# Optimization experiments

Measured on AMD Instinct MI355X. Metric: run time of the kernel, lower is better.

Reference implementation:

```python
import jax, jax.numpy as jnp
import numpy as np

NUM_STEPS = 100
STEP = 2.0 / (NUM_STEPS - 1)          # bin width over [-1, 1]
EPS = 1.0 / NUM_STEPS
TSIZE = NUM_STEPS                      # bin centers t_k = -1 + k*STEP, k=0..99
B, D = 4096, 128
NUM_CLASSES = 100


def setup_inputs() -> dict:
    key = jax.random.key(0)
    k1, k2 = jax.random.split(key)
    embeddings = jax.random.normal(k1, (B, D), dtype=jnp.float32)
    classes = jax.random.randint(k2, (B,), 0, NUM_CLASSES)
    return {"embeddings": embeddings, "classes": classes}


def _histogram_loss(embeddings, classes):
    n = embeddings.shape[0]
    iu, ju = np.triu_indices(n, 1)            # static upper-triangular pair indices
    # cosine similarity of all pairs (outer_cosine_similarity)
    en = embeddings / jnp.linalg.norm(embeddings, axis=1, keepdims=True)
    dists = en @ en.T                          # [B, B]
    s = jnp.clip(dists[iu, ju], -1.0 + 1e-6, 1.0 - 1e-6)   # [P]
    pos = (classes[iu] == classes[ju])         # [P] bool

    # soft triangular-kernel 2-bin scatter (equivalent to indsa/indsb masking):
    # bin j gets (t_j + STEP - s)/STEP, bin j+1 gets (s - t_j)/STEP
    j = jnp.floor((s + 1.0 - 1e-6) / STEP).astype(jnp.int32)   # lower bin index
    t_j = j.astype(s.dtype) * STEP - 1.0
    w_hi = (s - t_j) / STEP                    # weight for bin j+1
    w_lo = (t_j + STEP - s) / STEP             # weight for bin j

    def histogram(mask):
        m = mask.astype(s.dtype)
        size = m.sum()
        h = jnp.zeros((TSIZE,), dtype=s.dtype)
        h = h.at[j].add(w_lo * m).at[j + 1].add(w_hi * m)
        return h / size

    hist_pos = histogram(pos)
    hist_neg = histogram(~pos)
    # tril-masked repeat + sum(0) in the original is exactly a cumulative sum
    hist_pos_cdf = jnp.cumsum(hist_pos)
    return jnp.sum(hist_neg * hist_pos_cdf)


def reference(embeddings, classes):
    return _histogram_loss(embeddings, classes)
```

## Files before the change

### kernel.cpp

```cpp
#include <hip/hip_runtime.h>
#include <hip/hip_bf16.h>
#include <cstddef>

#define BN 4096
#define DD 128
#define NSTEPS 100
#define PTILE 128
#define PLSTR 136
#define GRID_T 32
#define NOFF 496
#define NBLK2 512
#define NREPH 16
#define NREPC2 8

typedef __attribute__((ext_vector_type(8))) short bf16x8;
typedef __attribute__((ext_vector_type(4))) float f32x4;

__device__ __forceinline__ void faddf(float* p, float v) { unsafeAtomicAdd(p, v); }

#define ZERON 166

__global__ __launch_bounds__(256) void hl_normalize(const float* __restrict__ emb,
                                                    ushort* __restrict__ out,
                                                    float* __restrict__ zero_blk) {
    if (blockIdx.x == 0 && threadIdx.x < ZERON) zero_blk[threadIdx.x] = 0.f;
    int w = threadIdx.x >> 6;
    int lane = threadIdx.x & 63;
    int row = (blockIdx.x << 2) + w;
    const float2 v = *(const float2*)(emb + (size_t)row * DD + 2 * lane);
    float ss = v.x * v.x + v.y * v.y;
    #pragma unroll
    for (int off = 32; off > 0; off >>= 1) ss += __shfl_xor(ss, off);
    float inv = 1.0f / sqrtf(ss);
    __hip_bfloat16 b0 = __float2bfloat16(v.x * inv);
    __hip_bfloat16 b1 = __float2bfloat16(v.y * inv);
    ushort2 pk;
    pk.x = *(ushort*)&b0;
    pk.y = *(ushort*)&b1;
    *(ushort2*)(out + (size_t)row * DD + 2 * lane) = pk;
}

__global__ __launch_bounds__(256) void hl_poscls(const ushort* __restrict__ nemb,
                                                 const int* __restrict__ cls,
                                                 float* __restrict__ gPos,
                                                 unsigned int* __restrict__ gDoneP,
                                                 float* __restrict__ gCdf) {
    const int c = blockIdx.x;
    __shared__ int idx[256];
    __shared__ int scan[256];
    __shared__ ushort As[64 * PLSTR];
    __shared__ ushort Bs[64 * PLSTR];
    __shared__ float hpos[NREPH * 101];
    __shared__ int mTot;
    __shared__ int lastFlag;
    const int tid = threadIdx.x;

    for (int i = tid; i < NREPH * 101; i += 256) hpos[i] = 0.f;

    const int base = tid * 16;
    int myCnt = 0;
    #pragma unroll
    for (int k = 0; k < 16; ++k) myCnt += (cls[base + k] == c);
    scan[tid] = myCnt;
    __syncthreads();
    for (int s = 1; s < 256; s <<= 1) {
        int v = (tid >= s) ? scan[tid - s] : 0;
        __syncthreads();
        scan[tid] += v;
        __syncthreads();
    }
    int w = scan[tid] - myCnt;
    if (tid == 255) mTot = scan[255] > 256 ? 256 : scan[255];
    #pragma unroll
    for (int k = 0; k < 16; ++k) {
        if (cls[base + k] == c && w < 256) { idx[w] = base + k; ++w; }
    }
    __syncthreads();
    const int m = mTot;
    const int nt = (m + 63) >> 6;

    constexpr float INVSTEP = 49.5f;
    constexpr float CLIPV = 1.0f - 1e-6f;

    const int lane = tid & 63;
    const int wv = tid >> 6;
    const int lr = lane & 15;
    const int kg = lane >> 4;
    const int rep = (lane & 15) * 101;

    for (int si = 0; si < nt; ++si) {
        for (int sj = si; sj < nt; ++sj) {
            __syncthreads();
            #pragma unroll
            for (int it = 0; it < 4; ++it) {
                int q = it * 256 + tid;
                int row = q >> 4;
                int ch = q & 15;
                int ga = si * 64 + row;
                int gb = sj * 64 + row;
                int ra = idx[ga < m ? ga : 0];
                int rb = idx[gb < m ? gb : 0];
                *(float4*)(&As[row * PLSTR + ch * 8]) =
                    *(const float4*)(nemb + (size_t)ra * DD + ch * 8);
                *(float4*)(&Bs[row * PLSTR + ch * 8]) =
                    *(const float4*)(nemb + (size_t)rb * DD + ch * 8);
            }
            __syncthreads();

            f32x4 zero4 = {0.f, 0.f, 0.f, 0.f};
            f32x4 pacc[4] = {zero4, zero4, zero4, zero4};
            #pragma unroll
            for (int ks = 0; ks < 4; ++ks) {
                bf16x8 af = *(const bf16x8*)(&As[(wv * 16 + lr) * PLSTR + ks * 32 + kg * 8]);
                #pragma unroll
                for (int fb = 0; fb < 4; ++fb) {
                    bf16x8 bf = *(const bf16x8*)(&Bs[(fb * 16 + lr) * PLSTR + ks * 32 + kg * 8]);
                    pacc[fb] = __builtin_amdgcn_mfma_f32_16x16x32_bf16(af, bf, pacc[fb], 0, 0, 0);
                }
            }

            #pragma unroll
            for (int fb = 0; fb < 4; ++fb) {
                const int gb = sj * 64 + fb * 16 + lr;
                #pragma unroll
                for (int j = 0; j < 4; ++j) {
                    const int ga = si * 64 + wv * 16 + kg * 4 + j;
                    if (ga < gb && gb < m) {
                        float s = pacc[fb][j];
                        s = fminf(fmaxf(s, -CLIPV), CLIPV);
                        float u = (s + CLIPV) * INVSTEP;
                        int jb = (int)u;
                        if (jb > 98) jb = 98;
                        float w_hi = u - (float)jb;
                        float w_lo = 1.0f - w_hi;
                        faddf(&hpos[rep + jb], w_lo);
                        faddf(&hpos[rep + jb + 1], w_hi);
                    }
                }
            }
        }
    }
    __syncthreads();
    if (tid < NSTEPS) {
        float v = 0.f;
        #pragma unroll
        for (int r = 0; r < NREPH; ++r) v += hpos[r * 101 + tid];
        if (v != 0.f) faddf(&gPos[tid], v);
    }
    __threadfence();
    if (tid == 0) {
        unsigned int tk = atomicAdd(gDoneP, 1u);
        lastFlag = (tk == NSTEPS - 1);
    }
    __syncthreads();
    if (lastFlag) {
        float v = (tid < NSTEPS)
            ? __hip_atomic_load(&gPos[tid], __ATOMIC_RELAXED, __HIP_MEMORY_SCOPE_AGENT) : 0.f;
        if (tid < 128) hpos[tid] = v;
        __syncthreads();
        for (int off = 1; off < 128; off <<= 1) {
            float x = 0.f;
            if (tid < 128 && tid >= off) x = hpos[tid - off];
            __syncthreads();
            if (tid < 128) hpos[tid] += x;
            __syncthreads();
        }
        const float invsp = 1.0f / hpos[NSTEPS - 1];
        if (tid < NSTEPS) gCdf[tid] = hpos[tid] * invsp;
    }
}

__global__ __launch_bounds__(256, 2) void hl_neg(const ushort* __restrict__ nemb,
                                                 const int* __restrict__ cls,
                                                 const float* __restrict__ gCdf,
                                                 float* __restrict__ gLoss,
                                                 float* __restrict__ gCnt,
                                                 unsigned int* __restrict__ gDone,
                                                 float* __restrict__ out) {
    __shared__ __align__(16) char arena[65536];
    ushort* As = (ushort*)arena;
    ushort* Bs = (ushort*)(arena + 32768);
    float* accL = (float*)arena;
    __shared__ float2 cdf2[NREPC2 * 101];
    __shared__ float red[8];
    __shared__ int clsA[PTILE], clsB[PTILE];

    const int tid = threadIdx.x;
    const int lane = tid & 63;
    const int wid = tid >> 6;
    const int wr = wid >> 1, wc = wid & 1;
    const int lr = lane & 15;
    const int kg = lane >> 4;

    int ti0, tj0, ti1 = 0, nu = 1;
    {
        int t = blockIdx.x;
        if (t < NOFF) {
            int ti = 0, rem = t;
            while (rem >= GRID_T - 1 - ti) { rem -= GRID_T - 1 - ti; ++ti; }
            ti0 = ti; tj0 = ti + 1 + rem;
        } else {
            int d = (t - NOFF) * 2;
            ti0 = tj0 = d; ti1 = d + 1; nu = 2;
        }
    }

    for (int i = tid; i < NREPC2 * NSTEPS; i += 256) {
        int r = i / NSTEPS, b = i - r * NSTEPS;
        float c0 = gCdf[b];
        float c1 = gCdf[(b < NSTEPS - 1) ? b + 1 : NSTEPS - 1];
        float2 cd; cd.x = c0; cd.y = c1 - c0;
        cdf2[r * 101 + b] = cd;
    }

    constexpr float INVSTEP = 49.5f;
    constexpr float CLIPV = 1.0f - 1e-6f;
    const float2* crep2 = &cdf2[(lane & 7) * 101];
    const int li_base = wr * 64 + (kg << 2);
    const int lj_base = wc * 64 + lr;

    float lacc = 0.f, lcnt = 0.f;
    const int rloc = lane >> 4;
    const int pch = lane & 15;

    for (int u = 0; u < nu; ++u) {
        const int ti = u ? ti1 : ti0;
        const int tj = u ? ti1 : tj0;
        const bool diag = (ti == tj);

        __syncthreads();
        if (tid < PTILE) clsA[tid] = cls[ti * PTILE + tid];
        else             clsB[tid - PTILE] = cls[tj * PTILE + (tid - PTILE)];

        {
            const ushort* Ag = nemb + (size_t)(ti * PTILE) * DD;
            const ushort* Bg = nemb + (size_t)(tj * PTILE) * DD;
            #pragma unroll
            for (int t = 0; t < 8; ++t) {
                int row = wid * 32 + t * 4 + rloc;
                int lch = pch ^ (row & 7);
                const ushort* ga = Ag + (size_t)row * DD + lch * 8;
                ushort* la = &As[(wid * 32 + t * 4) * 128];
                __builtin_amdgcn_global_load_lds(
                    (const __attribute__((address_space(1))) void*)ga,
                    (__attribute__((address_space(3))) void*)la, 16, 0, 0);
            }
            if (!diag) {
                #pragma unroll
                for (int t = 0; t < 8; ++t) {
                    int row = wid * 32 + t * 4 + rloc;
                    int lch = pch ^ (row & 7);
                    const ushort* gb = Bg + (size_t)row * DD + lch * 8;
                    ushort* lb = &Bs[(wid * 32 + t * 4) * 128];
                    __builtin_amdgcn_global_load_lds(
                        (const __attribute__((address_space(1))) void*)gb,
                        (__attribute__((address_space(3))) void*)lb, 16, 0, 0);
                }
            }
        }
        __syncthreads();

        const ushort* Bsel = diag ? As : Bs;
        const int* clsBsel = diag ? clsA : clsB;

        f32x4 zero4 = {0.f, 0.f, 0.f, 0.f};
        f32x4 acc[4][4];
        #pragma unroll
        for (int a = 0; a < 4; ++a)
            #pragma unroll
            for (int b = 0; b < 4; ++b) acc[a][b] = zero4;

        #pragma unroll
        for (int ks = 0; ks < 4; ++ks) {
            bf16x8 af[4], bfr[4];
            #pragma unroll
            for (int f = 0; f < 4; ++f) {
                int arow = wr * 64 + f * 16 + lr;
                int pca = ((ks << 2) | kg) ^ (arow & 7);
                af[f] = *(const bf16x8*)(&As[arow * 128 + pca * 8]);
                int brow = wc * 64 + f * 16 + lr;
                int pcb = ((ks << 2) | kg) ^ (brow & 7);
                bfr[f] = *(const bf16x8*)(&Bsel[brow * 128 + pcb * 8]);
            }
            #pragma unroll
            for (int fa = 0; fa < 4; ++fa)
                #pragma unroll
                for (int fb = 0; fb < 4; ++fb)
                    acc[fa][fb] = __builtin_amdgcn_mfma_f32_16x16x32_bf16(af[fa], bfr[fb], acc[fa][fb], 0, 0, 0);
        }

        __syncthreads();

        #pragma unroll
        for (int fb = 0; fb < 4; ++fb)
            #pragma unroll
            for (int fa = 0; fa < 4; ++fa)
                #pragma unroll
                for (int j = 0; j < 4; ++j)
                    accL[(fb * 16 + fa * 4 + j) * 256 + tid] = acc[fa][fb][j];
        __syncthreads();

        const bool offdiag = !diag;
        #pragma unroll 1
        for (int p = 0; p < 64; ++p) {
            const int fb = p >> 4, fa = (p >> 2) & 3, j = p & 3;
            const int li = li_base + fa * 16 + j;
            const int lj = lj_base + fb * 16;
            float s = accL[p * 256 + tid];
            int ca = clsA[li];
            int cb = clsBsel[lj];
            const bool mneg = (offdiag || (li < lj)) && (ca != cb);
            s = fminf(fmaxf(s, -CLIPV), CLIPV);
            float uu = (s + CLIPV) * INVSTEP;
            int jb = (int)uu;
            if (jb > 98) jb = 98;
            float w_hi = uu - (float)jb;
            float2 cd = crep2[jb];
            float mm = mneg ? 1.0f : 0.0f;
            lacc = fmaf(mm, fmaf(w_hi, cd.y, cd.x), lacc);
            lcnt += mm;
        }
    }

    #pragma unroll
    for (int off = 32; off > 0; off >>= 1) {
        lacc += __shfl_xor(lacc, off);
        lcnt += __shfl_xor(lcnt, off);
    }
    if (lane == 0) { red[wid] = lacc; red[4 + wid] = lcnt; }
    __syncthreads();
    if (tid == 0) {
        float L = red[0] + red[1] + red[2] + red[3];
        float C = red[4] + red[5] + red[6] + red[7];
        faddf(&gLoss[blockIdx.x & 31], L);
        faddf(&gCnt[blockIdx.x & 31], C);
        __threadfence();
        unsigned int tk = atomicAdd(gDone, 1u);
        if (tk == NBLK2 - 1) {
            __threadfence();
            float ls = 0.f, cs = 0.f;
            for (int i = 0; i < 32; ++i) {
                ls += __hip_atomic_load(&gLoss[i], __ATOMIC_RELAXED, __HIP_MEMORY_SCOPE_AGENT);
                cs += __hip_atomic_load(&gCnt[i], __ATOMIC_RELAXED, __HIP_MEMORY_SCOPE_AGENT);
            }
            out[0] = ls / cs;
        }
    }
}

extern "C" void kernel_launch(void* const* d_in, const int* in_sizes, int n_in,
                              void* d_out, int out_size, void* d_ws, size_t ws_size,
                              hipStream_t stream) {
    const float* emb = (const float*)d_in[0];
    const int* classes = (const int*)d_in[1];
    float* out = (float*)d_out;

    ushort* nemb = (ushort*)d_ws;
    float* ctl = (float*)((char*)d_ws + (size_t)BN * DD * sizeof(ushort));
    float* gPos = ctl;
    float* gLoss = gPos + NSTEPS;
    float* gCnt = gLoss + 32;
    unsigned int* gDone = (unsigned int*)(gCnt + 32);
    unsigned int* gDoneP = gDone + 1;
    float* gCdf = (float*)(gDoneP + 1);

    hl_normalize<<<BN / 4, 256, 0, stream>>>(emb, nemb, ctl);
    hl_poscls<<<NSTEPS, 256, 0, stream>>>(nemb, classes, gPos, gDoneP, gCdf);
    hl_neg<<<NBLK2, 256, 0, stream>>>(nemb, classes, gCdf, gLoss, gCnt, gDone, out);
}
```

Measured before the change: 51.64 us.

## Process two tile pairs per block, prefetch second tile, epilogue from registers

Each hl_neg block now handles two tile-pair units, with the grid halved to 264 blocks. The second unit's global-to-LDS loads are issued right after the first unit's MFMAs finish, so they overlap the first unit's epilogue. The epilogue reads similarities straight from the MFMA accumulator registers instead of spilling them to LDS and re-reading, which removes one barrier and the LDS round trip. The cost is more register pressure and fewer blocks, which with 256 CUs leaves roughly one block per CU.

```diff
diff --git a/kernel.cpp b/kernel.cpp
--- a/kernel.cpp
+++ b/kernel.cpp
@@ -9,7 +9,8 @@
 #define PLSTR 136
 #define GRID_T 32
 #define NOFF 496
-#define NBLK2 512
+#define NUNITS 528
+#define NBLK 264
 #define NREPH 16
 #define NREPC2 8
 
@@ -177,13 +178,11 @@
                                                  float* __restrict__ gCnt,
                                                  unsigned int* __restrict__ gDone,
                                                  float* __restrict__ out) {
-    __shared__ __align__(16) char arena[65536];
-    ushort* As = (ushort*)arena;
-    ushort* Bs = (ushort*)(arena + 32768);
-    float* accL = (float*)arena;
+    __shared__ ushort As[PTILE * 128];
+    __shared__ ushort Bs[PTILE * 128];
     __shared__ float2 cdf2[NREPC2 * 101];
     __shared__ float red[8];
-    __shared__ int clsA[PTILE], clsB[PTILE];
+    __shared__ int clsAb[2][PTILE], clsBb[2][PTILE];
 
     const int tid = threadIdx.x;
     const int lane = tid & 63;
@@ -192,16 +191,16 @@
     const int lr = lane & 15;
     const int kg = lane >> 4;
 
-    int ti0, tj0, ti1 = 0, nu = 1;
-    {
-        int t = blockIdx.x;
-        if (t < NOFF) {
-            int ti = 0, rem = t;
+    int tiU[2], tjU[2];
+    #pragma unroll
+    for (int u = 0; u < 2; ++u) {
+        int id = blockIdx.x * 2 + u;
+        if (id < NOFF) {
+            int ti = 0, rem = id;
             while (rem >= GRID_T - 1 - ti) { rem -= GRID_T - 1 - ti; ++ti; }
-            ti0 = ti; tj0 = ti + 1 + rem;
+            tiU[u] = ti; tjU[u] = ti + 1 + rem;
         } else {
-            int d = (t - NOFF) * 2;
-            ti0 = tj0 = d; ti1 = d + 1; nu = 2;
+            tiU[u] = tjU[u] = id - NOFF;
         }
     }
 
@@ -223,45 +222,47 @@
     const int rloc = lane >> 4;
     const int pch = lane & 15;
 
-    for (int u = 0; u < nu; ++u) {
-        const int ti = u ? ti1 : ti0;
-        const int tj = u ? ti1 : tj0;
-        const bool diag = (ti == tj);
-
-        __syncthreads();
-        if (tid < PTILE) clsA[tid] = cls[ti * PTILE + tid];
-        else             clsB[tid - PTILE] = cls[tj * PTILE + (tid - PTILE)];
-
-        {
-            const ushort* Ag = nemb + (size_t)(ti * PTILE) * DD;
-            const ushort* Bg = nemb + (size_t)(tj * PTILE) * DD;
-            #pragma unroll
-            for (int t = 0; t < 8; ++t) {
-                int row = wid * 32 + t * 4 + rloc;
-                int lch = pch ^ (row & 7);
-                const ushort* ga = Ag + (size_t)row * DD + lch * 8;
-                ushort* la = &As[(wid * 32 + t * 4) * 128];
-                __builtin_amdgcn_global_load_lds(
-                    (const __attribute__((address_space(1))) void*)ga,
-                    (__attribute__((address_space(3))) void*)la, 16, 0, 0);
-            }
-            if (!diag) {
-                #pragma unroll
-                for (int t = 0; t < 8; ++t) {
-                    int row = wid * 32 + t * 4 + rloc;
-                    int lch = pch ^ (row & 7);
-                    const ushort* gb = Bg + (size_t)row * DD + lch * 8;
-                    ushort* lb = &Bs[(wid * 32 + t * 4) * 128];
-                    __builtin_amdgcn_global_load_lds(
-                        (const __attribute__((address_space(1))) void*)gb,
-                        (__attribute__((address_space(3))) void*)lb, 16, 0, 0);
-                }
-            }
-        }
+    #define STAGE_UNIT(U)                                                            \
+    {                                                                                \
+        const int ti_ = tiU[U], tj_ = tjU[U];                                        \
+        const bool dg_ = (ti_ == tj_);                                               \
+        if (tid < PTILE) clsAb[(U) & 1][tid] = cls[ti_ * PTILE + tid];               \
+        else             clsBb[(U) & 1][tid - PTILE] = cls[tj_ * PTILE + (tid - PTILE)]; \
+        const ushort* Ag_ = nemb + (size_t)(ti_ * PTILE) * DD;                       \
+        const ushort* Bg_ = nemb + (size_t)(tj_ * PTILE) * DD;                       \
+        _Pragma("unroll")                                                            \
+        for (int t = 0; t < 8; ++t) {                                                \
+            int row = wid * 32 + t * 4 + rloc;                                       \
+            int lch = pch ^ (row & 7);                                               \
+            const ushort* ga = Ag_ + (size_t)row * DD + lch * 8;                     \
+            ushort* la = &As[(wid * 32 + t * 4) * 128];                              \
+            __builtin_amdgcn_global_load_lds(                                        \
+                (const __attribute__((address_space(1))) void*)ga,                   \
+                (__attribute__((address_space(3))) void*)la, 16, 0, 0);              \
+        }                                                                            \
+        if (!dg_) {                                                                  \
+            _Pragma("unroll")                                                        \
+            for (int t = 0; t < 8; ++t) {                                            \
+                int row = wid * 32 + t * 4 + rloc;                                   \
+                int lch = pch ^ (row & 7);                                           \
+                const ushort* gb = Bg_ + (size_t)row * DD + lch * 8;                 \
+                ushort* lb = &Bs[(wid * 32 + t * 4) * 128];                          \
+                __builtin_amdgcn_global_load_lds(                                    \
+                    (const __attribute__((address_space(1))) void*)gb,               \
+                    (__attribute__((address_space(3))) void*)lb, 16, 0, 0);          \
+            }                                                                        \
+        }                                                                            \
+    }
+
+    STAGE_UNIT(0);
+
+    #pragma unroll
+    for (int u = 0; u < 2; ++u) {
+        const bool diag = (tiU[u] == tjU[u]);
+
         __syncthreads();
 
         const ushort* Bsel = diag ? As : Bs;
-        const int* clsBsel = diag ? clsA : clsB;
 
         f32x4 zero4 = {0.f, 0.f, 0.f, 0.f};
         f32x4 acc[4][4];
@@ -291,36 +292,45 @@
 
         __syncthreads();
 
-        #pragma unroll
-        for (int fb = 0; fb < 4; ++fb)
-            #pragma unroll
-            for (int fa = 0; fa < 4; ++fa)
+        if (u == 0) STAGE_UNIT(1);
+
+        const int* clsA_ = clsAb[u & 1];
+        const int* clsB_ = diag ? clsAb[u & 1] : clsBb[u & 1];
+        const bool offdiag = !diag;
+
+        int ca[16];
+        #pragma unroll
+        for (int fa = 0; fa < 4; ++fa)
+            #pragma unroll
+            for (int j = 0; j < 4; ++j) ca[fa * 4 + j] = clsA_[li_base + fa * 16 + j];
+
+        #pragma unroll
+        for (int fb = 0; fb < 4; ++fb) {
+            const int lj = lj_base + fb * 16;
+            const int cb = clsB_[lj];
+            #pragma unroll
+            for (int fa = 0; fa < 4; ++fa) {
+                const int li0 = li_base + fa * 16;
+                f32x4 v = acc[fa][fb];
                 #pragma unroll
-                for (int j = 0; j < 4; ++j)
-                    accL[(fb * 16 + fa * 4 + j) * 256 + tid] = acc[fa][fb][j];
-        __syncthreads();
-
-        const bool offdiag = !diag;
-        #pragma unroll 1
-        for (int p = 0; p < 64; ++p) {
-            const int fb = p >> 4, fa = (p >> 2) & 3, j = p & 3;
-            const int li = li_base + fa * 16 + j;
-            const int lj = lj_base + fb * 16;
-            float s = accL[p * 256 + tid];
-            int ca = clsA[li];
-            int cb = clsBsel[lj];
-            const bool mneg = (offdiag || (li < lj)) && (ca != cb);
-            s = fminf(fmaxf(s, -CLIPV), CLIPV);
-            float uu = (s + CLIPV) * INVSTEP;
-            int jb = (int)uu;
-            if (jb > 98) jb = 98;
-            float w_hi = uu - (float)jb;
-            float2 cd = crep2[jb];
-            float mm = mneg ? 1.0f : 0.0f;
-            lacc = fmaf(mm, fmaf(w_hi, cd.y, cd.x), lacc);
-            lcnt += mm;
-        }
-    }
+                for (int j = 0; j < 4; ++j) {
+                    const int li = li0 + j;
+                    const bool mneg = (offdiag || (li < lj)) && (ca[fa * 4 + j] != cb);
+                    float s = v[j];
+                    s = fminf(fmaxf(s, -CLIPV), CLIPV);
+                    float uu = (s + CLIPV) * INVSTEP;
+                    int jb = (int)uu;
+                    if (jb > 98) jb = 98;
+                    float w_hi = uu - (float)jb;
+                    float2 cd = crep2[jb];
+                    float mm = mneg ? 1.0f : 0.0f;
+                    lacc = fmaf(mm, fmaf(w_hi, cd.y, cd.x), lacc);
+                    lcnt += mm;
+                }
+            }
+        }
+    }
+    #undef STAGE_UNIT
 
     #pragma unroll
     for (int off = 32; off > 0; off >>= 1) {
@@ -336,7 +346,7 @@
         faddf(&gCnt[blockIdx.x & 31], C);
         __threadfence();
         unsigned int tk = atomicAdd(gDone, 1u);
-        if (tk == NBLK2 - 1) {
+        if (tk == NBLK - 1) {
             __threadfence();
             float ls = 0.f, cs = 0.f;
             for (int i = 0; i < 32; ++i) {
@@ -366,5 +376,5 @@
 
     hl_normalize<<<BN / 4, 256, 0, stream>>>(emb, nemb, ctl);
     hl_poscls<<<NSTEPS, 256, 0, stream>>>(nemb, classes, gPos, gDoneP, gCdf);
-    hl_neg<<<NBLK2, 256, 0, stream>>>(nemb, classes, gCdf, gLoss, gCnt, gDone, out);
+    hl_neg<<<NBLK, 256, 0, stream>>>(nemb, classes, gCdf, gLoss, gCnt, gDone, out);
 }
```

Result: faster. 42.00 us (-18.7%).
